# Performance work log

Measured on AMD Instinct MI355X. Metric: run time of the kernel, lower is better.

## Reference

```python
import jax, jax.numpy as jnp
import numpy as np

T, IN, H = 16384, 1024, 4096   # tokens, in_features, hidden_features
G = 64                          # quantization group size (nunchaku default)
R = 32                          # LoRA rank for SVDQuant low-rank branch


def _dequant_weight(qw, ws):
    # qw: [out, in] int4 values in [-8,7] (stored int32); ws: [out, in//G] per-group scales
    out, inn = qw.shape
    w = qw.astype(jnp.float32).reshape(out, inn // G, G) * ws[:, :, None]
    return w.reshape(out, inn)


def _qdq_act(x):
    # simulate per-token, per-group int4 quantize->dequantize of activations
    t, d = x.shape
    xg = x.reshape(t, d // G, G)
    s = jnp.maximum(jnp.max(jnp.abs(xg), axis=-1, keepdims=True), 1e-6) / 7.0
    q = jnp.clip(jnp.round(xg / s), -8.0, 7.0)
    return (q * s).reshape(t, d)


def _svdquant_linear(x, qw, ws, smooth, ld, lu, b):
    # quantized main branch on smoothed input + full-precision LoRA correction on raw input
    xq = _qdq_act(x / smooth)                      # [T, d_in]
    w = _dequant_weight(qw, ws)                    # [d_out, d_in]
    main = jnp.einsum('td,od->to', xq, w)          # int4-sim GEMM
    lora = jnp.einsum('tr,or->to', jnp.einsum('td,rd->tr', x, ld), lu)
    return main + lora + b


def setup_inputs() -> dict:
    key = jax.random.key(0)
    ks = jax.random.split(key, 12)
    x = jax.random.normal(ks[0], (T, IN), dtype=jnp.float32)
    qw1 = jax.random.randint(ks[1], (H, IN), -8, 8, dtype=jnp.int32)
    ws1 = jax.random.uniform(ks[2], (H, IN // G), dtype=jnp.float32) * 0.01 + 0.001
    smooth1 = jax.random.uniform(ks[3], (IN,), dtype=jnp.float32) + 0.5
    ld1 = jax.random.normal(ks[4], (R, IN), dtype=jnp.float32) * 0.02
    lu1 = jax.random.normal(ks[5], (H, R), dtype=jnp.float32) * 0.02
    b1 = jax.random.normal(ks[6], (H,), dtype=jnp.float32) * 0.01
    qw2 = jax.random.randint(ks[7], (IN, H), -8, 8, dtype=jnp.int32)
    ws2 = jax.random.uniform(ks[8], (IN, H // G), dtype=jnp.float32) * 0.01 + 0.001
    smooth2 = jax.random.uniform(ks[9], (H,), dtype=jnp.float32) + 0.5
    ld2 = jax.random.normal(ks[10], (R, H), dtype=jnp.float32) * 0.02
    lu2 = jax.random.normal(ks[11], (IN, R), dtype=jnp.float32) * 0.02
    b2 = jnp.zeros((IN,), dtype=jnp.float32)
    return {"x": x, "qw1": qw1, "ws1": ws1, "smooth1": smooth1, "ld1": ld1,
            "lu1": lu1, "b1": b1, "qw2": qw2, "ws2": ws2, "smooth2": smooth2,
            "ld2": ld2, "lu2": lu2, "b2": b2}


def reference(x, qw1, ws1, smooth1, ld1, lu1, b1, qw2, ws2, smooth2, ld2, lu2, b2):
    h = _svdquant_linear(x, qw1, ws1, smooth1, ld1, lu1, b1)   # fc1
    h = jax.nn.gelu(h, approximate=True)                        # fused GELU
    y = _svdquant_linear(h, qw2, ws2, smooth2, ld2, lu2, b2)   # fc2
    return y
```

## Files before the change

kernel.cpp:

```cpp
#include <hip/hip_runtime.h>
#include <math.h>

#define T_TOK 16384
#define D_IN  1024
#define D_H   4096
#define GQ    64
#define R_L   32
#define NPANEL 4
#define PANW   (D_H / NPANEL)

typedef __attribute__((ext_vector_type(8))) __bf16 bf16x8;
typedef __attribute__((ext_vector_type(4))) float  f32x4;
typedef __attribute__((ext_vector_type(8))) unsigned short ushort8;

__device__ __forceinline__ unsigned short f2bf(float f) {
  union { float f; unsigned u; } v; v.f = f;
  unsigned u = v.u + 0x7FFFu + ((v.u >> 16) & 1u);
  return (unsigned short)(u >> 16);
}

__device__ __forceinline__ float bf2f(unsigned short h) {
  union { unsigned u; float f; } v; v.u = ((unsigned)h) << 16; return v.f;
}

__device__ __forceinline__ void gload_lds16(const unsigned short* g, unsigned short* l) {
  __builtin_amdgcn_global_load_lds(
      (const __attribute__((address_space(1))) unsigned int*)g,
      (__attribute__((address_space(3))) unsigned int*)l, 16, 0, 0);
}

__device__ __forceinline__ float gelu_tanh(float v) {
  float u = 0.7978845608028654f * (v + 0.044715f * v * v * v);
  return 0.5f * v * (1.0f + tanhf(u));
}

__global__ __launch_bounds__(256)
void convert_kernel(const int* __restrict__ qw1, const int* __restrict__ qw2,
                    unsigned short* __restrict__ qw1b, unsigned short* __restrict__ qw2b) {
  const size_t N1 = (size_t)D_H * D_IN;
  const size_t N2 = (size_t)D_IN * D_H;
  const size_t total = N1 + N2;
  for (size_t i = (size_t)blockIdx.x * 256 + threadIdx.x; i < total;
       i += (size_t)gridDim.x * 256) {
    if (i < N1) qw1b[i]    = f2bf((float)qw1[i]);
    else        qw2b[i-N1] = f2bf((float)qw2[i-N1]);
  }
}

__global__ __launch_bounds__(256)
void prep1_kernel(const float* __restrict__ x, const float* __restrict__ smooth,
                  const float* __restrict__ ld,
                  unsigned short* __restrict__ qx, float* __restrict__ sx,
                  float* __restrict__ xrf) {
  __shared__ float xrow[D_IN];
  const int t = blockIdx.x;
  const int tid = threadIdx.x;
  float4 x4  = *(const float4*)(x + (size_t)t * D_IN + tid * 4);
  float4 sm4 = *(const float4*)(smooth + tid * 4);
  *(float4*)&xrow[tid * 4] = x4;
  double z0 = (double)x4.x / (double)sm4.x;
  double z1 = (double)x4.y / (double)sm4.y;
  double z2 = (double)x4.z / (double)sm4.z;
  double z3 = (double)x4.w / (double)sm4.w;
  double amax = fmax(fmax(fabs(z0), fabs(z1)), fmax(fabs(z2), fabs(z3)));
#pragma unroll
  for (int d = 1; d < 16; d <<= 1) amax = fmax(amax, __shfl_xor(amax, d, 16));
  double s = fmax(amax, 1e-6) / 7.0;
  double q0 = fmin(fmax(rint(z0 / s), -8.0), 7.0);
  double q1 = fmin(fmax(rint(z1 / s), -8.0), 7.0);
  double q2 = fmin(fmax(rint(z2 / s), -8.0), 7.0);
  double q3 = fmin(fmax(rint(z3 / s), -8.0), 7.0);
  ushort4 qu; qu.x = f2bf((float)q0); qu.y = f2bf((float)q1);
  qu.z = f2bf((float)q2); qu.w = f2bf((float)q3);
  *(ushort4*)(qx + (size_t)t * D_IN + tid * 4) = qu;
  if ((tid & 15) == 0) sx[(size_t)t * (D_IN / GQ) + (tid >> 4)] = (float)s;
  __syncthreads();
  const int w = tid >> 6, l = tid & 63;
#pragma unroll
  for (int rr = 0; rr < 8; ++rr) {
    int r = w * 8 + rr;
    const float* ldr = ld + (size_t)r * D_IN;
    float sum = 0.f;
#pragma unroll
    for (int k = 0; k < 16; ++k)
      sum = fmaf(xrow[l + 64 * k], ldr[l + 64 * k], sum);
#pragma unroll
    for (int d = 32; d >= 1; d >>= 1) sum += __shfl_xor(sum, d, 64);
    if (l == 0) xrf[(size_t)t * R_L + r] = sum;
  }
}

__global__ __launch_bounds__(256, 2)
void gemm_fc1(const unsigned short* __restrict__ Aq,
              const float* __restrict__ Asx,
              const unsigned short* __restrict__ Bq,
              const float* __restrict__ Bws,
              const float* __restrict__ xrf,
              const float* __restrict__ lu1,
              const float* __restrict__ b1,
              const float* __restrict__ smooth2,
              int c0base,
              unsigned short* __restrict__ hb,
              unsigned short* __restrict__ qx2,
              float* __restrict__ sx2) {
  __shared__ __align__(16) char smem[36864];
  unsigned short* As = (unsigned short*)smem;
  unsigned short* Bs = (unsigned short*)(smem + 16384);
  float* sxs = (float*)(smem + 32768);
  float* wss = (float*)(smem + 33280);
  const int tid = threadIdx.x;
  const int lane = tid & 63;
  const int wid = tid >> 6;
  const int wr = wid >> 1, wc = wid & 1;
  const int l15 = lane & 15, l4 = lane >> 4;
  const int lin = blockIdx.y * 8 + blockIdx.x;
  const int sw  = (lin & 7) * 128 + (lin >> 3);
  const int t0 = (sw >> 3) * 128;
  const int c0 = c0base + (sw & 7) * 128;

  f32x4 acc[4][4] = {};
  const int srow = tid >> 3;
  const int ske  = (tid & 7) * 8;

  for (int g = 0; g < 16; ++g) {
    const int kA = g * 64 + ske;
#pragma unroll
    for (int i = 0; i < 4; ++i) {
      int row = i * 32 + srow;
      gload_lds16(Aq + (long)(t0 + row) * D_IN + kA, As + row * 64 + ske);
      gload_lds16(Bq + (long)(c0 + row) * D_IN + kA, Bs + row * 64 + ske);
    }
    if (tid < 128) sxs[tid] = Asx[(long)(t0 + tid) * 16 + g];
    else           wss[tid - 128] = Bws[(long)(c0 + tid - 128) * 16 + g];
    __syncthreads();

    bf16x8 af[4][2], bfr[4][2];
#pragma unroll
    for (int m = 0; m < 4; ++m) {
      const unsigned short* base = As + (wr * 64 + m * 16 + l15) * 64 + l4 * 8;
      af[m][0] = *(const bf16x8*)(base);
      af[m][1] = *(const bf16x8*)(base + 32);
    }
#pragma unroll
    for (int n = 0; n < 4; ++n) {
      const unsigned short* base = Bs + (wc * 64 + n * 16 + l15) * 64 + l4 * 8;
      bfr[n][0] = *(const bf16x8*)(base);
      bfr[n][1] = *(const bf16x8*)(base + 32);
    }
    f32x4 rsv[4];
#pragma unroll
    for (int m = 0; m < 4; ++m) rsv[m] = *(const f32x4*)&sxs[wr * 64 + m * 16 + l4 * 4];
    float csv[4];
#pragma unroll
    for (int n = 0; n < 4; ++n) csv[n] = wss[wc * 64 + n * 16 + l15];

#pragma unroll
    for (int m = 0; m < 4; ++m) {
#pragma unroll
      for (int n = 0; n < 4; ++n) {
        f32x4 t = {0.f, 0.f, 0.f, 0.f};
        t = __builtin_amdgcn_mfma_f32_16x16x32_bf16(af[m][0], bfr[n][0], t, 0, 0, 0);
        t = __builtin_amdgcn_mfma_f32_16x16x32_bf16(af[m][1], bfr[n][1], t, 0, 0, 0);
#pragma unroll
        for (int j = 0; j < 4; ++j)
          acc[m][n][j] = fmaf(t[j], rsv[m][j] * csv[n], acc[m][n][j]);
      }
    }
    __syncthreads();
  }

  float* xr_lds = (float*)smem;
  float* lu_lds = (float*)(smem + 18432);
  {
    const int row = tid >> 1;
    const int q4  = (tid & 1) * 16;
#pragma unroll
    for (int h = 0; h < 4; ++h) {
      *(float4*)&xr_lds[row * 36 + q4 + h * 4] =
          *(const float4*)(xrf + (size_t)(t0 + row) * R_L + q4 + h * 4);
      *(float4*)&lu_lds[row * 36 + q4 + h * 4] =
          *(const float4*)(lu1 + (size_t)(c0 + row) * R_L + q4 + h * 4);
    }
  }
  __syncthreads();

  float bv[4], rsmv[4];
  int colL[4];
#pragma unroll
  for (int n = 0; n < 4; ++n) {
    int col = c0 + wc * 64 + n * 16 + l15;
    colL[n] = wc * 64 + n * 16 + l15;
    bv[n] = b1[col];
    rsmv[n] = 1.0f / smooth2[col];
  }
  const int clocal0 = c0 - c0base;

#pragma unroll
  for (int m = 0; m < 4; ++m) {
#pragma unroll
    for (int j = 0; j < 4; ++j) {
      const int rloc = wr * 64 + m * 16 + l4 * 4 + j;
      const int trow = t0 + rloc;
      float lor[4] = {0.f, 0.f, 0.f, 0.f};
#pragma unroll
      for (int k = 0; k < 8; ++k) {
        const float4 xq = *(const float4*)&xr_lds[rloc * 36 + k * 4];
#pragma unroll
        for (int n = 0; n < 4; ++n) {
          const float4 lc = *(const float4*)&lu_lds[colL[n] * 36 + k * 4];
          lor[n] = fmaf(xq.x, lc.x, lor[n]);
          lor[n] = fmaf(xq.y, lc.y, lor[n]);
          lor[n] = fmaf(xq.z, lc.z, lor[n]);
          lor[n] = fmaf(xq.w, lc.w, lor[n]);
        }
      }
      float hv[4], z[4];
      float amax = 0.f;
#pragma unroll
      for (int n = 0; n < 4; ++n) {
        float v = acc[m][n][j] + lor[n] + bv[n];
        v = gelu_tanh(v);
        hv[n] = v;
        z[n] = v * rsmv[n];
        amax = fmaxf(amax, fabsf(z[n]));
      }
#pragma unroll
      for (int d = 1; d < 16; d <<= 1) amax = fmaxf(amax, __shfl_xor(amax, d, 16));
      float s = fmaxf(amax, 1e-6f) / 7.0f;
      float rs = 1.0f / s;
#pragma unroll
      for (int n = 0; n < 4; ++n) {
        int coll = clocal0 + wc * 64 + n * 16 + l15;
        hb[(size_t)trow * PANW + coll] = f2bf(hv[n]);
        float qv = fminf(fmaxf(rintf(z[n] * rs), -8.f), 7.f);
        qx2[(size_t)trow * PANW + coll] = f2bf(qv);
      }
      if (l15 == 0)
        sx2[(size_t)trow * (PANW / GQ) + ((clocal0 + wc * 64) >> 6)] = s;
    }
  }
}

__global__ __launch_bounds__(256, 2)
void gemm_fc2(const unsigned short* __restrict__ Aq,
              const float* __restrict__ Asx,
              const unsigned short* __restrict__ Bq,
              int kB0,
              const float* __restrict__ Bws,
              int gB0,
              float* __restrict__ Yout, int first) {
  __shared__ unsigned short As[128 * 64];
  __shared__ unsigned short Bs[128 * 64];
  __shared__ float sxs[128];
  __shared__ float wss[128];
  const int tid = threadIdx.x;
  const int lane = tid & 63;
  const int wid = tid >> 6;
  const int wr = wid >> 1, wc = wid & 1;
  const int l15 = lane & 15, l4 = lane >> 4;
  const int lin = blockIdx.y * 8 + blockIdx.x;
  const int sw  = (lin & 7) * 128 + (lin >> 3);
  const int t0 = (sw >> 3) * 128;
  const int c0 = (sw & 7) * 128;

  f32x4 acc[4][4] = {};
  const int srow = tid >> 3;
  const int ske = (tid & 7) * 8;

  for (int g = 0; g < 16; ++g) {
    const int kA = g * 64 + ske;
    const int kB = kB0 + kA;
#pragma unroll
    for (int i = 0; i < 4; ++i) {
      int row = i * 32 + srow;
      gload_lds16(Aq + (long)(t0 + row) * PANW + kA, As + row * 64 + ske);
      gload_lds16(Bq + (long)(c0 + row) * D_H + kB, Bs + row * 64 + ske);
    }
    if (tid < 128) sxs[tid] = Asx[(long)(t0 + tid) * (PANW / GQ) + g];
    else           wss[tid - 128] = Bws[(long)(c0 + tid - 128) * (D_H / GQ) + gB0 + g];
    __syncthreads();

    bf16x8 af[4][2], bfr[4][2];
#pragma unroll
    for (int m = 0; m < 4; ++m) {
      const unsigned short* base = As + (wr * 64 + m * 16 + l15) * 64 + l4 * 8;
      af[m][0] = *(const bf16x8*)(base);
      af[m][1] = *(const bf16x8*)(base + 32);
    }
#pragma unroll
    for (int n = 0; n < 4; ++n) {
      const unsigned short* base = Bs + (wc * 64 + n * 16 + l15) * 64 + l4 * 8;
      bfr[n][0] = *(const bf16x8*)(base);
      bfr[n][1] = *(const bf16x8*)(base + 32);
    }
    f32x4 rsv[4];
#pragma unroll
    for (int m = 0; m < 4; ++m) rsv[m] = *(const f32x4*)&sxs[wr * 64 + m * 16 + l4 * 4];
    float csv[4];
#pragma unroll
    for (int n = 0; n < 4; ++n) csv[n] = wss[wc * 64 + n * 16 + l15];

#pragma unroll
    for (int m = 0; m < 4; ++m) {
#pragma unroll
      for (int n = 0; n < 4; ++n) {
        f32x4 t = {0.f, 0.f, 0.f, 0.f};
        t = __builtin_amdgcn_mfma_f32_16x16x32_bf16(af[m][0], bfr[n][0], t, 0, 0, 0);
        t = __builtin_amdgcn_mfma_f32_16x16x32_bf16(af[m][1], bfr[n][1], t, 0, 0, 0);
#pragma unroll
        for (int j = 0; j < 4; ++j)
          acc[m][n][j] += t[j] * (rsv[m][j] * csv[n]);
      }
    }
    __syncthreads();
  }

#pragma unroll
  for (int m = 0; m < 4; ++m)
#pragma unroll
    for (int n = 0; n < 4; ++n) {
      int col = c0 + wc * 64 + n * 16 + l15;
#pragma unroll
      for (int j = 0; j < 4; ++j) {
        int trow = t0 + wr * 64 + m * 16 + l4 * 4 + j;
        size_t idx = (size_t)trow * D_IN + col;
        float v = acc[m][n][j];
        if (!first) v += Yout[idx];
        Yout[idx] = v;
      }
    }
}

__global__ __launch_bounds__(256)
void xr2_simple(const unsigned short* __restrict__ hp,
                const float* __restrict__ ld2,
                int c0base,
                float* __restrict__ xracc,
                int first) {
  __shared__ unsigned short hs[8][PANW + 8];
  const int tid = threadIdx.x;
  const int t0 = blockIdx.x * 8;
#pragma unroll
  for (int q = 0; q < 4; ++q) {
    int v = tid + 256 * q;
    int row = v >> 7;
    int col = (v & 127) * 8;
    *(ushort8*)(&hs[row][col]) =
        *(const ushort8*)(hp + (size_t)(t0 + row) * PANW + col);
  }
  __syncthreads();
  const int tloc = tid & 7;
  const int r    = tid >> 3;
  const float* ldr = ld2 + (size_t)r * D_H + c0base;
  float sum = 0.f;
  for (int k8 = 0; k8 < PANW / 8; ++k8) {
    ushort8 hv = *(const ushort8*)(&hs[tloc][k8 * 8]);
    float4 w0 = *(const float4*)(ldr + k8 * 8);
    float4 w1 = *(const float4*)(ldr + k8 * 8 + 4);
    sum = fmaf(bf2f(hv[0]), w0.x, sum);
    sum = fmaf(bf2f(hv[1]), w0.y, sum);
    sum = fmaf(bf2f(hv[2]), w0.z, sum);
    sum = fmaf(bf2f(hv[3]), w0.w, sum);
    sum = fmaf(bf2f(hv[4]), w1.x, sum);
    sum = fmaf(bf2f(hv[5]), w1.y, sum);
    sum = fmaf(bf2f(hv[6]), w1.z, sum);
    sum = fmaf(bf2f(hv[7]), w1.w, sum);
  }
  size_t idx = (size_t)(t0 + tloc) * R_L + r;
  xracc[idx] = (first ? 0.f : xracc[idx]) + sum;
}

__global__ __launch_bounds__(256)
void finish_kernel(const float* __restrict__ xracc,
                   const float* __restrict__ lu2,
                   const float* __restrict__ b2,
                   float* __restrict__ Yout) {
  __shared__ float xls[16][R_L];
  const int tid = threadIdx.x;
  const int o   = blockIdx.x * 256 + tid;
  const int t0r = blockIdx.y * 16;
  for (int q = tid; q < 16 * R_L; q += 256)
    xls[q >> 5][q & 31] = xracc[(size_t)(t0r + (q >> 5)) * R_L + (q & 31)];
  float lr[R_L];
#pragma unroll
  for (int r = 0; r < R_L; ++r) lr[r] = lu2[(size_t)o * R_L + r];
  const float b2v = b2[o];
  __syncthreads();
#pragma unroll
  for (int i = 0; i < 16; ++i) {
    size_t idx = (size_t)(t0r + i) * D_IN + o;
    float v = Yout[idx] + b2v;
#pragma unroll
    for (int r = 0; r < R_L; ++r) v = fmaf(lr[r], xls[i][r], v);
    Yout[idx] = v;
  }
}

extern "C" void kernel_launch(void* const* d_in, const int* in_sizes, int n_in,
                              void* d_out, int out_size, void* d_ws, size_t ws_size,
                              hipStream_t stream) {
  const float* x       = (const float*)d_in[0];
  const int*   qw1     = (const int*)d_in[1];
  const float* ws1     = (const float*)d_in[2];
  const float* smooth1 = (const float*)d_in[3];
  const float* ld1     = (const float*)d_in[4];
  const float* lu1     = (const float*)d_in[5];
  const float* b1      = (const float*)d_in[6];
  const int*   qw2     = (const int*)d_in[7];
  const float* ws2     = (const float*)d_in[8];
  const float* smooth2 = (const float*)d_in[9];
  const float* ld2     = (const float*)d_in[10];
  const float* lu2     = (const float*)d_in[11];
  const float* b2      = (const float*)d_in[12];

  char* w = (char*)d_ws;
  size_t off = 0;
  auto take = [&](size_t bytes) {
    char* p = w + off;
    off = (off + bytes + 255) & ~(size_t)255;
    return p;
  };

  unsigned short* qw1b = (unsigned short*)take((size_t)D_H * D_IN * 2);
  unsigned short* qw2b = (unsigned short*)take((size_t)D_IN * D_H * 2);
  unsigned short* qx1  = (unsigned short*)take((size_t)T_TOK * D_IN * 2);
  float*          sx1  = (float*)take((size_t)T_TOK * (D_IN / GQ) * 4);
  float*          xr1f = (float*)take((size_t)T_TOK * R_L * 4);
  unsigned short* hp   = (unsigned short*)take((size_t)T_TOK * PANW * 2);
  unsigned short* qx2p = (unsigned short*)take((size_t)T_TOK * PANW * 2);
  float*          sx2  = (float*)take((size_t)T_TOK * (PANW / GQ) * 4);
  float*          xr2a = (float*)take((size_t)T_TOK * R_L * 4);
  (void)ws_size; (void)in_sizes; (void)n_in; (void)out_size;

  convert_kernel<<<2048, 256, 0, stream>>>(qw1, qw2, qw1b, qw2b);
  prep1_kernel<<<T_TOK, 256, 0, stream>>>(x, smooth1, ld1, qx1, sx1, xr1f);

  for (int p = 0; p < NPANEL; ++p) {
    const int c0base = p * PANW;
    const int first = (p == 0);

    dim3 g1(PANW / 128, T_TOK / 128);
    gemm_fc1<<<g1, 256, 0, stream>>>(qx1, sx1, qw1b, ws1, xr1f, lu1, b1, smooth2,
                                     c0base, hp, qx2p, sx2);

    xr2_simple<<<T_TOK / 8, 256, 0, stream>>>(hp, ld2, c0base, xr2a, first);

    dim3 g2(D_IN / 128, T_TOK / 128);
    gemm_fc2<<<g2, 256, 0, stream>>>(qx2p, sx2, qw2b, c0base, ws2, p * (PANW / GQ),
                                     (float*)d_out, first);
  }

  dim3 gf(D_IN / 256, T_TOK / 16);
  finish_kernel<<<gf, 256, 0, stream>>>(xr2a, lu2, b2, (float*)d_out);
}
```

Before: 1.204 ms.

## Compute fc1 LoRA up-projection via split-bf16 MFMA and use fast GELU

Replaces the scalar FP32 LoRA up-projection in the fc1 epilogue, which staged xr and lu1 through LDS, with three bf16 MFMAs per tile (hi*hi, hi*lo, lo*hi) accumulating directly into the GEMM accumulators. xr and lu1 are pre-split into hi/lo bf16 pairs in the prep and convert kernels. GELU's tanhf is replaced with an __expf-based formula. The split-bf16 scheme and fast exp trade some precision for fewer ALU instructions and no LDS round trip in the epilogue.

New measurement: 1.133 ms. -5.9%, faster.

```diff
diff --git a/kernel.cpp b/kernel.cpp
--- a/kernel.cpp
+++ b/kernel.cpp
@@ -23,27 +23,42 @@
   union { unsigned u; float f; } v; v.u = ((unsigned)h) << 16; return v.f;
 }
 
+__device__ __forceinline__ void split_bf(float v, unsigned short* hi, unsigned short* lo) {
+  unsigned short h = f2bf(v);
+  *hi = h;
+  *lo = f2bf(v - bf2f(h));
+}
+
 __device__ __forceinline__ void gload_lds16(const unsigned short* g, unsigned short* l) {
   __builtin_amdgcn_global_load_lds(
       (const __attribute__((address_space(1))) unsigned int*)g,
       (__attribute__((address_space(3))) unsigned int*)l, 16, 0, 0);
 }
 
-__device__ __forceinline__ float gelu_tanh(float v) {
+__device__ __forceinline__ float gelu_fast(float v) {
   float u = 0.7978845608028654f * (v + 0.044715f * v * v * v);
-  return 0.5f * v * (1.0f + tanhf(u));
+  float e = __expf(2.0f * u);
+  float t = 1.0f - 2.0f / (e + 1.0f);
+  return 0.5f * v * (1.0f + t);
 }
 
 __global__ __launch_bounds__(256)
 void convert_kernel(const int* __restrict__ qw1, const int* __restrict__ qw2,
-                    unsigned short* __restrict__ qw1b, unsigned short* __restrict__ qw2b) {
+                    const float* __restrict__ lu1,
+                    unsigned short* __restrict__ qw1b, unsigned short* __restrict__ qw2b,
+                    unsigned short* __restrict__ lu1h, unsigned short* __restrict__ lu1l) {
   const size_t N1 = (size_t)D_H * D_IN;
   const size_t N2 = (size_t)D_IN * D_H;
-  const size_t total = N1 + N2;
+  const size_t N3 = (size_t)D_H * R_L;
+  const size_t total = N1 + N2 + N3;
   for (size_t i = (size_t)blockIdx.x * 256 + threadIdx.x; i < total;
        i += (size_t)gridDim.x * 256) {
-    if (i < N1) qw1b[i]    = f2bf((float)qw1[i]);
-    else        qw2b[i-N1] = f2bf((float)qw2[i-N1]);
+    if (i < N1)         qw1b[i]    = f2bf((float)qw1[i]);
+    else if (i < N1+N2) qw2b[i-N1] = f2bf((float)qw2[i-N1]);
+    else {
+      size_t j = i - N1 - N2;
+      split_bf(lu1[j], &lu1h[j], &lu1l[j]);
+    }
   }
 }
 
@@ -51,7 +66,7 @@
 void prep1_kernel(const float* __restrict__ x, const float* __restrict__ smooth,
                   const float* __restrict__ ld,
                   unsigned short* __restrict__ qx, float* __restrict__ sx,
-                  float* __restrict__ xrf) {
+                  unsigned short* __restrict__ xrh, unsigned short* __restrict__ xrl) {
   __shared__ float xrow[D_IN];
   const int t = blockIdx.x;
   const int tid = threadIdx.x;
@@ -86,7 +101,7 @@
       sum = fmaf(xrow[l + 64 * k], ldr[l + 64 * k], sum);
 #pragma unroll
     for (int d = 32; d >= 1; d >>= 1) sum += __shfl_xor(sum, d, 64);
-    if (l == 0) xrf[(size_t)t * R_L + r] = sum;
+    if (l == 0) split_bf(sum, &xrh[(size_t)t * R_L + r], &xrl[(size_t)t * R_L + r]);
   }
 }
 
@@ -95,19 +110,20 @@
               const float* __restrict__ Asx,
               const unsigned short* __restrict__ Bq,
               const float* __restrict__ Bws,
-              const float* __restrict__ xrf,
-              const float* __restrict__ lu1,
+              const unsigned short* __restrict__ xrh,
+              const unsigned short* __restrict__ xrl,
+              const unsigned short* __restrict__ luh,
+              const unsigned short* __restrict__ lul,
               const float* __restrict__ b1,
               const float* __restrict__ smooth2,
               int c0base,
               unsigned short* __restrict__ hb,
               unsigned short* __restrict__ qx2,
               float* __restrict__ sx2) {
-  __shared__ __align__(16) char smem[36864];
-  unsigned short* As = (unsigned short*)smem;
-  unsigned short* Bs = (unsigned short*)(smem + 16384);
-  float* sxs = (float*)(smem + 32768);
-  float* wss = (float*)(smem + 33280);
+  __shared__ unsigned short As[128 * 64];
+  __shared__ unsigned short Bs[128 * 64];
+  __shared__ float sxs[128];
+  __shared__ float wss[128];
   const int tid = threadIdx.x;
   const int lane = tid & 63;
   const int wid = tid >> 6;
@@ -169,27 +185,34 @@
     __syncthreads();
   }
 
-  float* xr_lds = (float*)smem;
-  float* lu_lds = (float*)(smem + 18432);
   {
-    const int row = tid >> 1;
-    const int q4  = (tid & 1) * 16;
-#pragma unroll
-    for (int h = 0; h < 4; ++h) {
-      *(float4*)&xr_lds[row * 36 + q4 + h * 4] =
-          *(const float4*)(xrf + (size_t)(t0 + row) * R_L + q4 + h * 4);
-      *(float4*)&lu_lds[row * 36 + q4 + h * 4] =
-          *(const float4*)(lu1 + (size_t)(c0 + row) * R_L + q4 + h * 4);
-    }
-  }
-  __syncthreads();
+    bf16x8 lah[4], lal[4], lbh[4], lbl[4];
+#pragma unroll
+    for (int m = 0; m < 4; ++m) {
+      size_t rb = (size_t)(t0 + wr * 64 + m * 16 + l15) * R_L + l4 * 8;
+      lah[m] = *(const bf16x8*)(xrh + rb);
+      lal[m] = *(const bf16x8*)(xrl + rb);
+    }
+#pragma unroll
+    for (int n = 0; n < 4; ++n) {
+      size_t rb = (size_t)(c0 + wc * 64 + n * 16 + l15) * R_L + l4 * 8;
+      lbh[n] = *(const bf16x8*)(luh + rb);
+      lbl[n] = *(const bf16x8*)(lul + rb);
+    }
+#pragma unroll
+    for (int m = 0; m < 4; ++m)
+#pragma unroll
+      for (int n = 0; n < 4; ++n) {
+        acc[m][n] = __builtin_amdgcn_mfma_f32_16x16x32_bf16(lah[m], lbh[n], acc[m][n], 0, 0, 0);
+        acc[m][n] = __builtin_amdgcn_mfma_f32_16x16x32_bf16(lah[m], lbl[n], acc[m][n], 0, 0, 0);
+        acc[m][n] = __builtin_amdgcn_mfma_f32_16x16x32_bf16(lal[m], lbh[n], acc[m][n], 0, 0, 0);
+      }
+  }
 
   float bv[4], rsmv[4];
-  int colL[4];
 #pragma unroll
   for (int n = 0; n < 4; ++n) {
     int col = c0 + wc * 64 + n * 16 + l15;
-    colL[n] = wc * 64 + n * 16 + l15;
     bv[n] = b1[col];
     rsmv[n] = 1.0f / smooth2[col];
   }
@@ -199,27 +222,12 @@
   for (int m = 0; m < 4; ++m) {
 #pragma unroll
     for (int j = 0; j < 4; ++j) {
-      const int rloc = wr * 64 + m * 16 + l4 * 4 + j;
-      const int trow = t0 + rloc;
-      float lor[4] = {0.f, 0.f, 0.f, 0.f};
-#pragma unroll
-      for (int k = 0; k < 8; ++k) {
-        const float4 xq = *(const float4*)&xr_lds[rloc * 36 + k * 4];
-#pragma unroll
-        for (int n = 0; n < 4; ++n) {
-          const float4 lc = *(const float4*)&lu_lds[colL[n] * 36 + k * 4];
-          lor[n] = fmaf(xq.x, lc.x, lor[n]);
-          lor[n] = fmaf(xq.y, lc.y, lor[n]);
-          lor[n] = fmaf(xq.z, lc.z, lor[n]);
-          lor[n] = fmaf(xq.w, lc.w, lor[n]);
-        }
-      }
+      const int trow = t0 + wr * 64 + m * 16 + l4 * 4 + j;
       float hv[4], z[4];
       float amax = 0.f;
 #pragma unroll
       for (int n = 0; n < 4; ++n) {
-        float v = acc[m][n][j] + lor[n] + bv[n];
-        v = gelu_tanh(v);
+        float v = gelu_fast(acc[m][n][j] + bv[n]);
         hv[n] = v;
         z[n] = v * rsmv[n];
         amax = fmaxf(amax, fabsf(z[n]));
@@ -423,25 +431,28 @@
 
   unsigned short* qw1b = (unsigned short*)take((size_t)D_H * D_IN * 2);
   unsigned short* qw2b = (unsigned short*)take((size_t)D_IN * D_H * 2);
+  unsigned short* lu1h = (unsigned short*)take((size_t)D_H * R_L * 2);
+  unsigned short* lu1l = (unsigned short*)take((size_t)D_H * R_L * 2);
   unsigned short* qx1  = (unsigned short*)take((size_t)T_TOK * D_IN * 2);
   float*          sx1  = (float*)take((size_t)T_TOK * (D_IN / GQ) * 4);
-  float*          xr1f = (float*)take((size_t)T_TOK * R_L * 4);
+  unsigned short* xr1h = (unsigned short*)take((size_t)T_TOK * R_L * 2);
+  unsigned short* xr1l = (unsigned short*)take((size_t)T_TOK * R_L * 2);
   unsigned short* hp   = (unsigned short*)take((size_t)T_TOK * PANW * 2);
   unsigned short* qx2p = (unsigned short*)take((size_t)T_TOK * PANW * 2);
   float*          sx2  = (float*)take((size_t)T_TOK * (PANW / GQ) * 4);
   float*          xr2a = (float*)take((size_t)T_TOK * R_L * 4);
   (void)ws_size; (void)in_sizes; (void)n_in; (void)out_size;
 
-  convert_kernel<<<2048, 256, 0, stream>>>(qw1, qw2, qw1b, qw2b);
-  prep1_kernel<<<T_TOK, 256, 0, stream>>>(x, smooth1, ld1, qx1, sx1, xr1f);
+  convert_kernel<<<2048, 256, 0, stream>>>(qw1, qw2, lu1, qw1b, qw2b, lu1h, lu1l);
+  prep1_kernel<<<T_TOK, 256, 0, stream>>>(x, smooth1, ld1, qx1, sx1, xr1h, xr1l);
 
   for (int p = 0; p < NPANEL; ++p) {
     const int c0base = p * PANW;
     const int first = (p == 0);
 
     dim3 g1(PANW / 128, T_TOK / 128);
-    gemm_fc1<<<g1, 256, 0, stream>>>(qx1, sx1, qw1b, ws1, xr1f, lu1, b1, smooth2,
-                                     c0base, hp, qx2p, sx2);
+    gemm_fc1<<<g1, 256, 0, stream>>>(qx1, sx1, qw1b, ws1, xr1h, xr1l, lu1h, lu1l,
+                                     b1, smooth2, c0base, hp, qx2p, sx2);
 
     xr2_simple<<<T_TOK / 8, 256, 0, stream>>>(hp, ld2, c0base, xr2a, first);
 
```
